# Kernel tuning notes

Measured on AMD Instinct MI355X. Metric: run time of the kernel, lower is better.

The kernel has to match this reference:

```python
import jax, jax.numpy as jnp
import numpy as np

N_NODES = 100000
N_EDGES = 1600000
D_IN, D_H, D_OUT = 128, 128, 64


def gcn_conv(x, src, dst, W, b, n_nodes):
    """PyG GCNConv (eval): x' = D^{-1/2} (A+I) D^{-1/2} X W + b.
    src/dst already include self-loops."""
    h = x @ W  # [N, d_out] -- transform first (fewer FLOPs when d_out <= d_in)
    deg = jax.ops.segment_sum(jnp.ones_like(dst, dtype=h.dtype), dst, num_segments=n_nodes)
    dinv = jnp.where(deg > 0, jax.lax.rsqrt(deg), 0.0)
    norm = dinv[src] * dinv[dst]  # [E]
    msg = h[src] * norm[:, None]  # gather + scale
    out = jax.ops.segment_sum(msg, dst, num_segments=n_nodes)  # scatter-add
    return out + b


def setup_inputs() -> dict:
    key = jax.random.key(0)
    k = jax.random.split(key, 8)
    x = jax.random.normal(k[0], (N_NODES, D_IN), dtype=jnp.float32)
    edge_index = jax.random.randint(k[1], (2, N_EDGES), 0, N_NODES, dtype=jnp.int32)
    s = 0.1
    W1 = jax.random.normal(k[2], (D_IN, D_H), dtype=jnp.float32) * s
    b1 = jnp.zeros((D_H,), dtype=jnp.float32)
    W2 = jax.random.normal(k[3], (D_H, D_H), dtype=jnp.float32) * s
    b2 = jnp.zeros((D_H,), dtype=jnp.float32)
    W3 = jax.random.normal(k[4], (D_H, D_OUT), dtype=jnp.float32) * s
    b3 = jnp.zeros((D_OUT,), dtype=jnp.float32)
    return {"x": x, "edge_index": edge_index, "W1": W1, "b1": b1,
            "W2": W2, "b2": b2, "W3": W3, "b3": b3}


def reference(x, edge_index, W1, b1, W2, b2, W3, b3):
    n = x.shape[0]
    # add self-loops once (shared by all layers)
    loops = jnp.arange(n, dtype=edge_index.dtype)
    src = jnp.concatenate([edge_index[0], loops])
    dst = jnp.concatenate([edge_index[1], loops])
    h = gcn_conv(x, src, dst, W1, b1, n)
    h = jax.nn.relu(h)  # dropout = identity in eval mode
    h = gcn_conv(h, src, dst, W2, b2, n)
    h = jax.nn.relu(h)
    out = gcn_conv(h, src, dst, W3, b3, n)
    return out
```

## Files before the change

### kernel.cpp

```cpp
#include <hip/hip_runtime.h>
#include <hip/hip_fp16.h>

#define N_NODES 100000
#define N_EDGES 1600000
#define NBUCKET 196
#define CAP     8960
#define EPB     6250

typedef _Float16 half8 __attribute__((ext_vector_type(8)));
typedef float float4v __attribute__((ext_vector_type(4)));

__launch_bounds__(256)
__global__ void k_partition(const int* __restrict__ src, const int* __restrict__ dst,
                            int* __restrict__ bcur, int* __restrict__ ebuf, int E) {
    __shared__ int hist[200];
    __shared__ int basebkt[200];
    const int tid = threadIdx.x;
    if (tid < 200) hist[tid] = 0;
    __syncthreads();
    const int e0 = blockIdx.x * EPB, e1 = min(e0 + EPB, E);
    for (int e = e0 + tid; e < e1; e += 256) atomicAdd(&hist[dst[e] >> 9], 1);
    __syncthreads();
    if (tid < NBUCKET) {
        int h = hist[tid];
        basebkt[tid] = tid * CAP + (h ? atomicAdd(&bcur[tid], h) : 0);
    }
    __syncthreads();
    if (tid < 200) hist[tid] = 0;
    __syncthreads();
    for (int e = e0 + tid; e < e1; e += 256) {
        int d = dst[e];
        int bk = d >> 9;
        int o = atomicAdd(&hist[bk], 1);
        ebuf[basebkt[bk] + o] = (src[e] << 9) | (d & 511);
    }
}

__launch_bounds__(256)
__global__ void k_bsort(const int* __restrict__ ebuf, const int* __restrict__ bcur,
                        int* __restrict__ adj, int* __restrict__ stv,
                        int* __restrict__ deg, float* __restrict__ dinv, int N) {
    __shared__ int cnt[512];
    __shared__ int offs[512];
    const int b = blockIdx.x;
    const int tid = threadIdx.x;
    const int base = b * CAP;
    const int n_b = min(bcur[b], CAP);
    const int node0 = b << 9;
    cnt[tid] = 0; cnt[tid + 256] = 0;
    __syncthreads();
    for (int i = tid; i < n_b; i += 256)
        atomicAdd(&cnt[ebuf[base + i] & 511], 1);
    __syncthreads();
    if (tid < 64) {
        int v[8], tot = 0;
#pragma unroll
        for (int j = 0; j < 8; ++j) { int t = cnt[tid * 8 + j]; v[j] = tot; tot += t; }
        int inc = tot;
#pragma unroll
        for (int d = 1; d < 64; d <<= 1) {
            int u = __shfl_up(inc, d, 64);
            if (tid >= d) inc += u;
        }
        const int excl = inc - tot;
#pragma unroll
        for (int j = 0; j < 8; ++j) offs[tid * 8 + j] = excl + v[j];
    }
    __syncthreads();
#pragma unroll
    for (int h = 0; h < 2; ++h) {
        int local = tid + h * 256;
        int node = node0 + local;
        if (node < N) {
            stv[node] = base + offs[local];
            deg[node] = cnt[local];
            dinv[node] = rsqrtf((float)(cnt[local] + 1));
        }
    }
    __syncthreads();
    for (int i = tid; i < n_b; i += 256) {
        int pk = ebuf[base + i];
        int pos = atomicAdd(&offs[pk & 511], 1);
        adj[base + pos] = pk >> 9;
    }
}

__global__ void k_wswz_all(const float* __restrict__ W1, const float* __restrict__ W2,
                           const float* __restrict__ W3, _Float16* __restrict__ wz1,
                           _Float16* __restrict__ wz2, _Float16* __restrict__ wz3,
                           int* __restrict__ bcur) {
    if (blockIdx.x == 0) bcur[threadIdx.x] = 0;
    int t = blockIdx.x * 256 + threadIdx.x;
    const float* W; _Float16* wsz; int BN;
    if (t < 2048)      { W = W1; wsz = wz1; BN = 128; }
    else if (t < 4096) { W = W2; wsz = wz2; BN = 128; t -= 2048; }
    else if (t < 5120) { W = W3; wsz = wz3; BN = 64;  t -= 4096; }
    else return;
    const int l = t & 63;
    const int kblk = (t >> 6) & 3;
    const int nt = t >> 8;
    const int krow = kblk * 32 + ((l >> 4) << 3);
    const int col = nt * 16 + (l & 15);
    _Float16 v[8];
#pragma unroll
    for (int j = 0; j < 8; ++j) v[j] = (_Float16)W[(krow + j) * BN + col];
    *(uint4*)&wsz[t << 3] = *(uint4*)v;
}

template <int BN, bool AFP16, int MINW>
__launch_bounds__(256, MINW)
__global__ void k_gemm_reg(const void* __restrict__ Xv, const _Float16* __restrict__ wsz,
                           const float* __restrict__ dinv, __half* __restrict__ out,
                           int N, int tiles) {
    constexpr int NT = BN / 16;
    const int lane = threadIdx.x & 63;
    const int q = lane >> 4;
    const int m = lane & 15;

    half8 wreg[NT * 4];
#pragma unroll
    for (int f = 0; f < NT * 4; ++f)
        wreg[f] = *(const half8*)&wsz[(f << 9) + (lane << 3)];

    const int wid = (blockIdx.x * 256 + threadIdx.x) >> 6;
    const int nw = gridDim.x * 4;

    for (int tile = wid; tile < tiles; tile += nw) {
        const int arow = tile * 16 + m;
        const int arowc = arow < N ? arow : N - 1;

        half8 xf[4];
        if constexpr (AFP16) {
            const _Float16* A = (const _Float16*)Xv + (size_t)arowc * 128 + (q << 3);
#pragma unroll
            for (int kb = 0; kb < 4; ++kb) xf[kb] = *(const half8*)(A + kb * 32);
        } else {
            const float* A = (const float*)Xv + (size_t)arowc * 128 + (q << 3);
#pragma unroll
            for (int kb = 0; kb < 4; ++kb) {
                float4 a0 = *(const float4*)(A + kb * 32);
                float4 a1 = *(const float4*)(A + kb * 32 + 4);
                xf[kb][0] = (_Float16)a0.x; xf[kb][1] = (_Float16)a0.y;
                xf[kb][2] = (_Float16)a0.z; xf[kb][3] = (_Float16)a0.w;
                xf[kb][4] = (_Float16)a1.x; xf[kb][5] = (_Float16)a1.y;
                xf[kb][6] = (_Float16)a1.z; xf[kb][7] = (_Float16)a1.w;
            }
        }

        float4v acc[NT];
#pragma unroll
        for (int nt = 0; nt < NT; ++nt) acc[nt] = (float4v){0.f, 0.f, 0.f, 0.f};
#pragma unroll
        for (int kb = 0; kb < 4; ++kb)
#pragma unroll
            for (int nt = 0; nt < NT; ++nt)
                acc[nt] = __builtin_amdgcn_mfma_f32_16x16x32_f16(wreg[nt * 4 + kb], xf[kb],
                                                                acc[nt], 0, 0, 0);

        if (arow < N) {
            const float s = dinv[arow];
#pragma unroll
            for (int nt = 0; nt < NT; ++nt) {
                _Float16 ov[4];
#pragma unroll
                for (int r = 0; r < 4; ++r) ov[r] = (_Float16)(acc[nt][r] * s);
                *(uint2*)&out[(size_t)arow * BN + nt * 16 + q * 4] = *(uint2*)ov;
            }
        }
    }
}

template <bool RELU>
__launch_bounds__(256)
__global__ void k_agg128(const __half* __restrict__ tp, const int* __restrict__ adj,
                         const int* __restrict__ startv, const int* __restrict__ deg,
                         const float* __restrict__ dinv, const float* __restrict__ bias,
                         _Float16* __restrict__ out, int N) {
    const int node = (blockIdx.x << 2) + (threadIdx.x >> 6);
    const int lane = threadIdx.x & 63;
    if (node >= N) return;
    const int s = startv[node];
    const int cnt = deg[node];
    const float di = dinv[node];
    const int g = lane >> 4;
    const int sl = lane & 15;
    const uint4* rowb = (const uint4*)tp;

    float acc[8] = {0.f, 0.f, 0.f, 0.f, 0.f, 0.f, 0.f, 0.f};
    auto addrow = [&](uint4 v) {
        float2 f0 = __half22float2(*(__half2*)&v.x);
        float2 f1 = __half22float2(*(__half2*)&v.y);
        float2 f2 = __half22float2(*(__half2*)&v.z);
        float2 f3 = __half22float2(*(__half2*)&v.w);
        acc[0] += f0.x; acc[1] += f0.y; acc[2] += f1.x; acc[3] += f1.y;
        acc[4] += f2.x; acc[5] += f2.y; acc[6] += f3.x; acc[7] += f3.y;
    };
    if (g == 0) addrow(rowb[(size_t)node * 16 + sl]);

    int e = 0;
    for (; e + 16 <= cnt; e += 16) {
        int j[4];
#pragma unroll
        for (int u = 0; u < 4; ++u) j[u] = adj[s + e + 4 * u + g];
        uint4 v[4];
#pragma unroll
        for (int u = 0; u < 4; ++u) v[u] = rowb[(size_t)j[u] * 16 + sl];
#pragma unroll
        for (int u = 0; u < 4; ++u) addrow(v[u]);
    }
    for (; e + 4 <= cnt; e += 4)
        addrow(rowb[(size_t)adj[s + e + g] * 16 + sl]);
    if (e + g < cnt)
        addrow(rowb[(size_t)adj[s + e + g] * 16 + sl]);

#pragma unroll
    for (int i = 0; i < 8; ++i) {
        acc[i] += __shfl_xor(acc[i], 32);
        acc[i] += __shfl_xor(acc[i], 16);
    }
    if (g == 0) {
        float4 b0 = *(const float4*)&bias[sl * 8];
        float4 b1 = *(const float4*)&bias[sl * 8 + 4];
        float o[8];
        o[0] = di * acc[0] + b0.x; o[1] = di * acc[1] + b0.y;
        o[2] = di * acc[2] + b0.z; o[3] = di * acc[3] + b0.w;
        o[4] = di * acc[4] + b1.x; o[5] = di * acc[5] + b1.y;
        o[6] = di * acc[6] + b1.z; o[7] = di * acc[7] + b1.w;
        if (RELU)
#pragma unroll
            for (int i = 0; i < 8; ++i) o[i] = fmaxf(o[i], 0.f);
        __half2 ov[4];
#pragma unroll
        for (int i = 0; i < 4; ++i) ov[i] = __floats2half2_rn(o[2 * i], o[2 * i + 1]);
        *(uint4*)&out[(size_t)node * 128 + sl * 8] = *(uint4*)ov;
    }
}

__launch_bounds__(256)
__global__ void k_agg64(const __half* __restrict__ tp, const int* __restrict__ adj,
                        const int* __restrict__ startv, const int* __restrict__ deg,
                        const float* __restrict__ dinv, const float* __restrict__ bias,
                        float* __restrict__ out, int N) {
    const int node = (blockIdx.x << 2) + (threadIdx.x >> 6);
    const int lane = threadIdx.x & 63;
    if (node >= N) return;
    const int s = startv[node];
    const int cnt = deg[node];
    const float di = dinv[node];
    const int g = lane >> 4;
    const int sl = lane & 15;
    const uint2* rowb = (const uint2*)tp;

    float acc[4] = {0.f, 0.f, 0.f, 0.f};
    auto addrow = [&](uint2 v) {
        float2 f0 = __half22float2(*(__half2*)&v.x);
        float2 f1 = __half22float2(*(__half2*)&v.y);
        acc[0] += f0.x; acc[1] += f0.y; acc[2] += f1.x; acc[3] += f1.y;
    };
    if (g == 0) addrow(rowb[(size_t)node * 16 + sl]);

    int e = 0;
    for (; e + 16 <= cnt; e += 16) {
        int j[4];
#pragma unroll
        for (int u = 0; u < 4; ++u) j[u] = adj[s + e + 4 * u + g];
        uint2 v[4];
#pragma unroll
        for (int u = 0; u < 4; ++u) v[u] = rowb[(size_t)j[u] * 16 + sl];
#pragma unroll
        for (int u = 0; u < 4; ++u) addrow(v[u]);
    }
    for (; e + 4 <= cnt; e += 4)
        addrow(rowb[(size_t)adj[s + e + g] * 16 + sl]);
    if (e + g < cnt)
        addrow(rowb[(size_t)adj[s + e + g] * 16 + sl]);

#pragma unroll
    for (int i = 0; i < 4; ++i) {
        acc[i] += __shfl_xor(acc[i], 32);
        acc[i] += __shfl_xor(acc[i], 16);
    }
    if (g == 0) {
        float4 bb = *(const float4*)&bias[sl * 4];
        float4 o;
        o.x = di * acc[0] + bb.x; o.y = di * acc[1] + bb.y;
        o.z = di * acc[2] + bb.z; o.w = di * acc[3] + bb.w;
        *(float4*)&out[(size_t)node * 64 + sl * 4] = o;
    }
}

extern "C" void kernel_launch(void* const* d_in, const int* in_sizes, int n_in,
                              void* d_out, int out_size, void* d_ws, size_t ws_size,
                              hipStream_t stream) {
    const float* x  = (const float*)d_in[0];
    const int*   ei = (const int*)d_in[1];
    const float* W1 = (const float*)d_in[2];
    const float* b1 = (const float*)d_in[3];
    const float* W2 = (const float*)d_in[4];
    const float* b2 = (const float*)d_in[5];
    const float* W3 = (const float*)d_in[6];
    const float* b3 = (const float*)d_in[7];
    float* out = (float*)d_out;
    const int* src = ei;
    const int* dst = ei + N_EDGES;

    char* p = (char*)d_ws;
    __half* tp      = (__half*)p;    p += (size_t)N_NODES * 128 * 2;
    _Float16* hbuf  = (_Float16*)p;  p += (size_t)N_NODES * 128 * 2;
    int*   deg  = (int*)p;    p += (size_t)N_NODES * 4;
    float* dinv = (float*)p;  p += (size_t)N_NODES * 4;
    int*   stv  = (int*)p;    p += (size_t)N_NODES * 4;
    int*   bCur = (int*)p;    p += 1024;
    int*   adj  = (int*)p;    p += (size_t)NBUCKET * CAP * 4 + 16384;
    _Float16* wz1 = (_Float16*)p; p += 16384 * 2;
    _Float16* wz2 = (_Float16*)p; p += 16384 * 2;
    _Float16* wz3 = (_Float16*)p; p += 8192 * 2;
    size_t need = (size_t)(p - (char*)d_ws);
    if (ws_size < need) return;

    int* ebuf = (int*)tp;

    k_wswz_all<<<20, 256, 0, stream>>>(W1, W2, W3, wz1, wz2, wz3, bCur);
    k_partition<<<256, 256, 0, stream>>>(src, dst, bCur, ebuf, N_EDGES);
    k_bsort<<<NBUCKET, 256, 0, stream>>>(ebuf, bCur, adj, stv, deg, dinv, N_NODES);

    const int tiles = (N_NODES + 15) / 16;
    const int ab = (N_NODES + 3) / 4;
    k_gemm_reg<128, false, 2><<<512, 256, 0, stream>>>(x, wz1, dinv, tp, N_NODES, tiles);
    k_agg128<true><<<ab, 256, 0, stream>>>(tp, adj, stv, deg, dinv, b1, hbuf, N_NODES);
    k_gemm_reg<128, true, 2><<<512, 256, 0, stream>>>(hbuf, wz2, dinv, tp, N_NODES, tiles);
    k_agg128<true><<<ab, 256, 0, stream>>>(tp, adj, stv, deg, dinv, b2, hbuf, N_NODES);
    k_gemm_reg<64, true, 4><<<1024, 256, 0, stream>>>(hbuf, wz3, dinv, tp, N_NODES, tiles);
    k_agg64<<<ab, 256, 0, stream>>>(tp, adj, stv, deg, dinv, b3, out, N_NODES);
}
```

Before: 367.9 us.

## Fuse all GCN stages into one persistent kernel with software grid barriers

Replaces the eight separate launches (weight swizzle, partition, bucket sort, three GEMMs, three aggregations) with a single persistent kernel of 1024 blocks. The stages are separated by a hierarchical atomic grid barrier, and the first GEMM overlaps with the bucket sort on the blocks left free. The source-side dinv scaling moves from the GEMM epilogue into the aggregation as a per-neighbor fma, which adds a dinv gather per edge. Weights are staged in LDS instead of registers. The change targets launch gaps and tail effects, but relies on all 1024 blocks being co-resident and a spin barrier with a timeout, which could deadlock or give wrong results if occupancy is insufficient.

```diff
diff --git a/kernel.cpp b/kernel.cpp
--- a/kernel.cpp
+++ b/kernel.cpp
@@ -5,130 +5,53 @@
 #define N_EDGES 1600000
 #define NBUCKET 196
 #define CAP     8960
-#define EPB     6250
+#define GRID    1024
+#define PBLK    (GRID - 20)
+#define EPB2    ((N_EDGES + PBLK - 1) / PBLK)
+#define NTILES  ((N_NODES + 15) / 16)
 
 typedef _Float16 half8 __attribute__((ext_vector_type(8)));
 typedef float float4v __attribute__((ext_vector_type(4)));
 
-__launch_bounds__(256)
-__global__ void k_partition(const int* __restrict__ src, const int* __restrict__ dst,
-                            int* __restrict__ bcur, int* __restrict__ ebuf, int E) {
-    __shared__ int hist[200];
-    __shared__ int basebkt[200];
+__device__ __forceinline__ void gridbar(int* bb, int phase) {
+    __syncthreads();
+    if (threadIdx.x == 0) {
+        __threadfence();
+        int g = blockIdx.x & 31;
+        if (atomicAdd(&bb[256 + phase * 32 + g], 1) == 31) {
+            if (atomicAdd(&bb[128 + phase * 16], 1) == 31) {
+                __threadfence();
+                atomicExch(&bb[phase * 16], 1);
+            }
+        }
+        long it = 0;
+        while (__hip_atomic_load(&bb[phase * 16], __ATOMIC_ACQUIRE,
+                                 __HIP_MEMORY_SCOPE_AGENT) == 0) {
+            __builtin_amdgcn_s_sleep(8);
+            if (++it > 1000000L) break;
+        }
+        __threadfence();
+    }
+    __syncthreads();
+}
+
+template <int BN, bool AFP16>
+__device__ __forceinline__ void gemm_phase(const void* Xv, const _Float16* wsz,
+                                           __half* out, _Float16* smem,
+                                           int bstart, int bcnt) {
+    if ((int)blockIdx.x < bstart) return;
     const int tid = threadIdx.x;
-    if (tid < 200) hist[tid] = 0;
+    for (int i = tid; i < BN * 16; i += 256)
+        *(uint4*)&smem[i << 3] = *(const uint4*)&wsz[i << 3];
     __syncthreads();
-    const int e0 = blockIdx.x * EPB, e1 = min(e0 + EPB, E);
-    for (int e = e0 + tid; e < e1; e += 256) atomicAdd(&hist[dst[e] >> 9], 1);
-    __syncthreads();
-    if (tid < NBUCKET) {
-        int h = hist[tid];
-        basebkt[tid] = tid * CAP + (h ? atomicAdd(&bcur[tid], h) : 0);
-    }
-    __syncthreads();
-    if (tid < 200) hist[tid] = 0;
-    __syncthreads();
-    for (int e = e0 + tid; e < e1; e += 256) {
-        int d = dst[e];
-        int bk = d >> 9;
-        int o = atomicAdd(&hist[bk], 1);
-        ebuf[basebkt[bk] + o] = (src[e] << 9) | (d & 511);
-    }
-}
-
-__launch_bounds__(256)
-__global__ void k_bsort(const int* __restrict__ ebuf, const int* __restrict__ bcur,
-                        int* __restrict__ adj, int* __restrict__ stv,
-                        int* __restrict__ deg, float* __restrict__ dinv, int N) {
-    __shared__ int cnt[512];
-    __shared__ int offs[512];
-    const int b = blockIdx.x;
-    const int tid = threadIdx.x;
-    const int base = b * CAP;
-    const int n_b = min(bcur[b], CAP);
-    const int node0 = b << 9;
-    cnt[tid] = 0; cnt[tid + 256] = 0;
-    __syncthreads();
-    for (int i = tid; i < n_b; i += 256)
-        atomicAdd(&cnt[ebuf[base + i] & 511], 1);
-    __syncthreads();
-    if (tid < 64) {
-        int v[8], tot = 0;
-#pragma unroll
-        for (int j = 0; j < 8; ++j) { int t = cnt[tid * 8 + j]; v[j] = tot; tot += t; }
-        int inc = tot;
-#pragma unroll
-        for (int d = 1; d < 64; d <<= 1) {
-            int u = __shfl_up(inc, d, 64);
-            if (tid >= d) inc += u;
-        }
-        const int excl = inc - tot;
-#pragma unroll
-        for (int j = 0; j < 8; ++j) offs[tid * 8 + j] = excl + v[j];
-    }
-    __syncthreads();
-#pragma unroll
-    for (int h = 0; h < 2; ++h) {
-        int local = tid + h * 256;
-        int node = node0 + local;
-        if (node < N) {
-            stv[node] = base + offs[local];
-            deg[node] = cnt[local];
-            dinv[node] = rsqrtf((float)(cnt[local] + 1));
-        }
-    }
-    __syncthreads();
-    for (int i = tid; i < n_b; i += 256) {
-        int pk = ebuf[base + i];
-        int pos = atomicAdd(&offs[pk & 511], 1);
-        adj[base + pos] = pk >> 9;
-    }
-}
-
-__global__ void k_wswz_all(const float* __restrict__ W1, const float* __restrict__ W2,
-                           const float* __restrict__ W3, _Float16* __restrict__ wz1,
-                           _Float16* __restrict__ wz2, _Float16* __restrict__ wz3,
-                           int* __restrict__ bcur) {
-    if (blockIdx.x == 0) bcur[threadIdx.x] = 0;
-    int t = blockIdx.x * 256 + threadIdx.x;
-    const float* W; _Float16* wsz; int BN;
-    if (t < 2048)      { W = W1; wsz = wz1; BN = 128; }
-    else if (t < 4096) { W = W2; wsz = wz2; BN = 128; t -= 2048; }
-    else if (t < 5120) { W = W3; wsz = wz3; BN = 64;  t -= 4096; }
-    else return;
-    const int l = t & 63;
-    const int kblk = (t >> 6) & 3;
-    const int nt = t >> 8;
-    const int krow = kblk * 32 + ((l >> 4) << 3);
-    const int col = nt * 16 + (l & 15);
-    _Float16 v[8];
-#pragma unroll
-    for (int j = 0; j < 8; ++j) v[j] = (_Float16)W[(krow + j) * BN + col];
-    *(uint4*)&wsz[t << 3] = *(uint4*)v;
-}
-
-template <int BN, bool AFP16, int MINW>
-__launch_bounds__(256, MINW)
-__global__ void k_gemm_reg(const void* __restrict__ Xv, const _Float16* __restrict__ wsz,
-                           const float* __restrict__ dinv, __half* __restrict__ out,
-                           int N, int tiles) {
-    constexpr int NT = BN / 16;
-    const int lane = threadIdx.x & 63;
+    const int lane = tid & 63;
     const int q = lane >> 4;
     const int m = lane & 15;
-
-    half8 wreg[NT * 4];
-#pragma unroll
-    for (int f = 0; f < NT * 4; ++f)
-        wreg[f] = *(const half8*)&wsz[(f << 9) + (lane << 3)];
-
-    const int wid = (blockIdx.x * 256 + threadIdx.x) >> 6;
-    const int nw = gridDim.x * 4;
-
-    for (int tile = wid; tile < tiles; tile += nw) {
+    const int wid = (((int)blockIdx.x - bstart) << 2) + (tid >> 6);
+    const int nw = bcnt << 2;
+    for (int tile = wid; tile < NTILES; tile += nw) {
         const int arow = tile * 16 + m;
-        const int arowc = arow < N ? arow : N - 1;
-
+        const int arowc = arow < N_NODES ? arow : N_NODES - 1;
         half8 xf[4];
         if constexpr (AFP16) {
             const _Float16* A = (const _Float16*)Xv + (size_t)arowc * 128 + (q << 3);
@@ -146,147 +69,223 @@
                 xf[kb][6] = (_Float16)a1.z; xf[kb][7] = (_Float16)a1.w;
             }
         }
-
+        constexpr int NT = BN / 16;
         float4v acc[NT];
 #pragma unroll
         for (int nt = 0; nt < NT; ++nt) acc[nt] = (float4v){0.f, 0.f, 0.f, 0.f};
 #pragma unroll
         for (int kb = 0; kb < 4; ++kb)
 #pragma unroll
-            for (int nt = 0; nt < NT; ++nt)
-                acc[nt] = __builtin_amdgcn_mfma_f32_16x16x32_f16(wreg[nt * 4 + kb], xf[kb],
-                                                                acc[nt], 0, 0, 0);
-
-        if (arow < N) {
-            const float s = dinv[arow];
+            for (int nt = 0; nt < NT; ++nt) {
+                half8 wf = *(const half8*)&smem[(((nt << 2) + kb) << 9) + (lane << 3)];
+                acc[nt] = __builtin_amdgcn_mfma_f32_16x16x32_f16(wf, xf[kb], acc[nt], 0, 0, 0);
+            }
+        if (arow < N_NODES) {
 #pragma unroll
             for (int nt = 0; nt < NT; ++nt) {
                 _Float16 ov[4];
 #pragma unroll
-                for (int r = 0; r < 4; ++r) ov[r] = (_Float16)(acc[nt][r] * s);
+                for (int r = 0; r < 4; ++r) ov[r] = (_Float16)acc[nt][r];
                 *(uint2*)&out[(size_t)arow * BN + nt * 16 + q * 4] = *(uint2*)ov;
             }
         }
     }
 }
 
-template <bool RELU>
-__launch_bounds__(256)
-__global__ void k_agg128(const __half* __restrict__ tp, const int* __restrict__ adj,
-                         const int* __restrict__ startv, const int* __restrict__ deg,
-                         const float* __restrict__ dinv, const float* __restrict__ bias,
-                         _Float16* __restrict__ out, int N) {
-    const int node = (blockIdx.x << 2) + (threadIdx.x >> 6);
+template <int D, bool RELU, typename OT>
+__device__ __forceinline__ void agg_phase(const __half* tp, const int* adj,
+                                          const int* stv, const int* deg,
+                                          const float* dinv, const float* bias,
+                                          OT* out) {
+    const int w = threadIdx.x >> 6;
     const int lane = threadIdx.x & 63;
-    if (node >= N) return;
-    const int s = startv[node];
-    const int cnt = deg[node];
-    const float di = dinv[node];
     const int g = lane >> 4;
     const int sl = lane & 15;
-    const uint4* rowb = (const uint4*)tp;
-
-    float acc[8] = {0.f, 0.f, 0.f, 0.f, 0.f, 0.f, 0.f, 0.f};
-    auto addrow = [&](uint4 v) {
-        float2 f0 = __half22float2(*(__half2*)&v.x);
-        float2 f1 = __half22float2(*(__half2*)&v.y);
-        float2 f2 = __half22float2(*(__half2*)&v.z);
-        float2 f3 = __half22float2(*(__half2*)&v.w);
-        acc[0] += f0.x; acc[1] += f0.y; acc[2] += f1.x; acc[3] += f1.y;
-        acc[4] += f2.x; acc[5] += f2.y; acc[6] += f3.x; acc[7] += f3.y;
-    };
-    if (g == 0) addrow(rowb[(size_t)node * 16 + sl]);
-
-    int e = 0;
-    for (; e + 16 <= cnt; e += 16) {
-        int j[4];
-#pragma unroll
-        for (int u = 0; u < 4; ++u) j[u] = adj[s + e + 4 * u + g];
-        uint4 v[4];
-#pragma unroll
-        for (int u = 0; u < 4; ++u) v[u] = rowb[(size_t)j[u] * 16 + sl];
-#pragma unroll
-        for (int u = 0; u < 4; ++u) addrow(v[u]);
-    }
-    for (; e + 4 <= cnt; e += 4)
-        addrow(rowb[(size_t)adj[s + e + g] * 16 + sl]);
-    if (e + g < cnt)
-        addrow(rowb[(size_t)adj[s + e + g] * 16 + sl]);
-
-#pragma unroll
-    for (int i = 0; i < 8; ++i) {
-        acc[i] += __shfl_xor(acc[i], 32);
-        acc[i] += __shfl_xor(acc[i], 16);
-    }
-    if (g == 0) {
-        float4 b0 = *(const float4*)&bias[sl * 8];
-        float4 b1 = *(const float4*)&bias[sl * 8 + 4];
-        float o[8];
-        o[0] = di * acc[0] + b0.x; o[1] = di * acc[1] + b0.y;
-        o[2] = di * acc[2] + b0.z; o[3] = di * acc[3] + b0.w;
-        o[4] = di * acc[4] + b1.x; o[5] = di * acc[5] + b1.y;
-        o[6] = di * acc[6] + b1.z; o[7] = di * acc[7] + b1.w;
-        if (RELU)
-#pragma unroll
-            for (int i = 0; i < 8; ++i) o[i] = fmaxf(o[i], 0.f);
-        __half2 ov[4];
-#pragma unroll
-        for (int i = 0; i < 4; ++i) ov[i] = __floats2half2_rn(o[2 * i], o[2 * i + 1]);
-        *(uint4*)&out[(size_t)node * 128 + sl * 8] = *(uint4*)ov;
-    }
-}
-
-__launch_bounds__(256)
-__global__ void k_agg64(const __half* __restrict__ tp, const int* __restrict__ adj,
-                        const int* __restrict__ startv, const int* __restrict__ deg,
-                        const float* __restrict__ dinv, const float* __restrict__ bias,
-                        float* __restrict__ out, int N) {
-    const int node = (blockIdx.x << 2) + (threadIdx.x >> 6);
-    const int lane = threadIdx.x & 63;
-    if (node >= N) return;
-    const int s = startv[node];
-    const int cnt = deg[node];
-    const float di = dinv[node];
-    const int g = lane >> 4;
-    const int sl = lane & 15;
-    const uint2* rowb = (const uint2*)tp;
-
-    float acc[4] = {0.f, 0.f, 0.f, 0.f};
-    auto addrow = [&](uint2 v) {
-        float2 f0 = __half22float2(*(__half2*)&v.x);
-        float2 f1 = __half22float2(*(__half2*)&v.y);
-        acc[0] += f0.x; acc[1] += f0.y; acc[2] += f1.x; acc[3] += f1.y;
-    };
-    if (g == 0) addrow(rowb[(size_t)node * 16 + sl]);
-
-    int e = 0;
-    for (; e + 16 <= cnt; e += 16) {
-        int j[4];
-#pragma unroll
-        for (int u = 0; u < 4; ++u) j[u] = adj[s + e + 4 * u + g];
-        uint2 v[4];
-#pragma unroll
-        for (int u = 0; u < 4; ++u) v[u] = rowb[(size_t)j[u] * 16 + sl];
-#pragma unroll
-        for (int u = 0; u < 4; ++u) addrow(v[u]);
-    }
-    for (; e + 4 <= cnt; e += 4)
-        addrow(rowb[(size_t)adj[s + e + g] * 16 + sl]);
-    if (e + g < cnt)
-        addrow(rowb[(size_t)adj[s + e + g] * 16 + sl]);
-
-#pragma unroll
-    for (int i = 0; i < 4; ++i) {
-        acc[i] += __shfl_xor(acc[i], 32);
-        acc[i] += __shfl_xor(acc[i], 16);
-    }
-    if (g == 0) {
-        float4 bb = *(const float4*)&bias[sl * 4];
-        float4 o;
-        o.x = di * acc[0] + bb.x; o.y = di * acc[1] + bb.y;
-        o.z = di * acc[2] + bb.z; o.w = di * acc[3] + bb.w;
-        *(float4*)&out[(size_t)node * 64 + sl * 4] = o;
-    }
+    constexpr int NA = D / 16;
+
+    for (int node = ((int)blockIdx.x << 2) + w; node < N_NODES; node += GRID * 4) {
+        const int s = stv[node];
+        const int cnt = deg[node];
+        const float di = dinv[node];
+        float acc[NA];
+#pragma unroll
+        for (int i = 0; i < NA; ++i) acc[i] = 0.f;
+
+        auto addrow = [&](float c, const __half2* v) {
+#pragma unroll
+            for (int i = 0; i < NA / 2; ++i) {
+                float2 f = __half22float2(v[i]);
+                acc[2 * i] = fmaf(c, f.x, acc[2 * i]);
+                acc[2 * i + 1] = fmaf(c, f.y, acc[2 * i + 1]);
+            }
+        };
+        const __half2* base = (const __half2*)tp;
+        if (g == 0) addrow(di, base + (size_t)node * (D / 2) + sl * (NA / 2));
+        int e = 0;
+        for (; e + 16 <= cnt; e += 16) {
+            int j[4];
+#pragma unroll
+            for (int u = 0; u < 4; ++u) j[u] = adj[s + e + 4 * u + g];
+            float dj[4];
+#pragma unroll
+            for (int u = 0; u < 4; ++u) dj[u] = dinv[j[u]];
+            __half2 v[4][NA / 2];
+#pragma unroll
+            for (int u = 0; u < 4; ++u)
+#pragma unroll
+                for (int i = 0; i < NA / 2; ++i)
+                    v[u][i] = base[(size_t)j[u] * (D / 2) + sl * (NA / 2) + i];
+#pragma unroll
+            for (int u = 0; u < 4; ++u) addrow(dj[u], v[u]);
+        }
+        for (; e + 4 <= cnt; e += 4) {
+            int j = adj[s + e + g];
+            addrow(dinv[j], base + (size_t)j * (D / 2) + sl * (NA / 2));
+        }
+        if (e + g < cnt) {
+            int j = adj[s + e + g];
+            addrow(dinv[j], base + (size_t)j * (D / 2) + sl * (NA / 2));
+        }
+#pragma unroll
+        for (int i = 0; i < NA; ++i) {
+            acc[i] += __shfl_xor(acc[i], 32);
+            acc[i] += __shfl_xor(acc[i], 16);
+        }
+        if (g == 0) {
+            float o[NA];
+#pragma unroll
+            for (int i = 0; i < NA; ++i) {
+                o[i] = di * acc[i] + bias[sl * NA + i];
+                if (RELU) o[i] = fmaxf(o[i], 0.f);
+            }
+            if constexpr (sizeof(OT) == 2) {
+                __half2 ov[NA / 2];
+#pragma unroll
+                for (int i = 0; i < NA / 2; ++i)
+                    ov[i] = __floats2half2_rn(o[2 * i], o[2 * i + 1]);
+                if constexpr (NA == 8)
+                    *(uint4*)&out[(size_t)node * D + sl * NA] = *(uint4*)ov;
+                else
+                    *(uint2*)&out[(size_t)node * D + sl * NA] = *(uint2*)ov;
+            } else {
+#pragma unroll
+                for (int i = 0; i < NA; i += 4)
+                    *(float4*)&out[(size_t)node * D + sl * NA + i] = *(float4*)&o[i];
+            }
+        }
+    }
+}
+
+__launch_bounds__(256, 4)
+__global__ void k_mega(const float* __restrict__ x, const int* __restrict__ src,
+                       const int* __restrict__ dst,
+                       const float* __restrict__ W1, const float* __restrict__ W2,
+                       const float* __restrict__ W3,
+                       const float* __restrict__ b1, const float* __restrict__ b2,
+                       const float* __restrict__ b3,
+                       int* bb, int* bCur, int* ebuf,
+                       _Float16* wz1, _Float16* wz2, _Float16* wz3,
+                       int* adj, int* stv, int* deg, float* dinv,
+                       __half* tp, _Float16* hbuf, float* out) {
+    __shared__ __align__(16) _Float16 smem[16384];
+    const int b = blockIdx.x;
+    const int tid = threadIdx.x;
+
+    if (b < 20) {
+        int t = b * 256 + tid;
+        const float* W; _Float16* wsz; int BN;
+        if (t < 2048)      { W = W1; wsz = wz1; BN = 128; }
+        else if (t < 4096) { W = W2; wsz = wz2; BN = 128; t -= 2048; }
+        else               { W = W3; wsz = wz3; BN = 64;  t -= 4096; }
+        const int l = t & 63;
+        const int kblk = (t >> 6) & 3;
+        const int nt = t >> 8;
+        const int krow = kblk * 32 + ((l >> 4) << 3);
+        const int col = nt * 16 + (l & 15);
+        _Float16 v[8];
+#pragma unroll
+        for (int j = 0; j < 8; ++j) v[j] = (_Float16)W[(krow + j) * BN + col];
+        *(uint4*)&wsz[t << 3] = *(uint4*)v;
+    } else {
+        int* hist = (int*)smem;
+        int* basebkt = hist + 256;
+        if (tid < 256) hist[tid] = 0;
+        __syncthreads();
+        const int e0 = (b - 20) * EPB2, e1 = min(e0 + EPB2, N_EDGES);
+        for (int e = e0 + tid; e < e1; e += 256) atomicAdd(&hist[dst[e] >> 9], 1);
+        __syncthreads();
+        if (tid < NBUCKET) {
+            int h = hist[tid];
+            basebkt[tid] = tid * CAP + (h ? atomicAdd(&bCur[tid], h) : 0);
+        }
+        __syncthreads();
+        if (tid < 256) hist[tid] = 0;
+        __syncthreads();
+        for (int e = e0 + tid; e < e1; e += 256) {
+            int d = dst[e];
+            int bk = d >> 9;
+            int o = atomicAdd(&hist[bk], 1);
+            ebuf[basebkt[bk] + o] = (src[e] << 9) | (d & 511);
+        }
+    }
+    gridbar(bb, 0);
+
+    if (b < NBUCKET) {
+        int* cnt = (int*)smem;
+        int* offs = cnt + 512;
+        const int base = b * CAP;
+        const int n_b = min(bCur[b], CAP);
+        const int node0 = b << 9;
+        cnt[tid] = 0; cnt[tid + 256] = 0;
+        __syncthreads();
+        for (int i = tid; i < n_b; i += 256)
+            atomicAdd(&cnt[ebuf[base + i] & 511], 1);
+        __syncthreads();
+        if (tid < 64) {
+            int v[8], tot = 0;
+#pragma unroll
+            for (int j = 0; j < 8; ++j) { int t = cnt[tid * 8 + j]; v[j] = tot; tot += t; }
+            int inc = tot;
+#pragma unroll
+            for (int d = 1; d < 64; d <<= 1) {
+                int u = __shfl_up(inc, d, 64);
+                if (tid >= d) inc += u;
+            }
+            const int excl = inc - tot;
+#pragma unroll
+            for (int j = 0; j < 8; ++j) offs[tid * 8 + j] = excl + v[j];
+        }
+        __syncthreads();
+#pragma unroll
+        for (int h = 0; h < 2; ++h) {
+            int local = tid + h * 256;
+            int node = node0 + local;
+            if (node < N_NODES) {
+                stv[node] = base + offs[local];
+                deg[node] = cnt[local];
+                dinv[node] = rsqrtf((float)(cnt[local] + 1));
+            }
+        }
+        __syncthreads();
+        for (int i = tid; i < n_b; i += 256) {
+            int pk = ebuf[base + i];
+            int pos = atomicAdd(&offs[pk & 511], 1);
+            adj[base + pos] = pk >> 9;
+        }
+    } else {
+        gemm_phase<128, false>(x, wz1, tp, smem, NBUCKET, GRID - NBUCKET);
+    }
+    gridbar(bb, 1);
+
+    agg_phase<128, true, _Float16>(tp, adj, stv, deg, dinv, b1, hbuf);
+    gridbar(bb, 2);
+    gemm_phase<128, true>(hbuf, wz2, tp, smem, 0, GRID);
+    gridbar(bb, 3);
+    agg_phase<128, true, _Float16>(tp, adj, stv, deg, dinv, b2, hbuf);
+    gridbar(bb, 4);
+    gemm_phase<64, true>(hbuf, wz3, tp, smem, 0, GRID);
+    gridbar(bb, 5);
+    agg_phase<64, false, float>(tp, adj, stv, deg, dinv, b3, out);
 }
 
 extern "C" void kernel_launch(void* const* d_in, const int* in_sizes, int n_in,
@@ -305,31 +304,23 @@
     const int* dst = ei + N_EDGES;
 
     char* p = (char*)d_ws;
+    int*  bb   = (int*)p;     p += 2048;
+    int*  bCur = (int*)p;     p += 2048;
     __half* tp      = (__half*)p;    p += (size_t)N_NODES * 128 * 2;
     _Float16* hbuf  = (_Float16*)p;  p += (size_t)N_NODES * 128 * 2;
     int*   deg  = (int*)p;    p += (size_t)N_NODES * 4;
     float* dinv = (float*)p;  p += (size_t)N_NODES * 4;
     int*   stv  = (int*)p;    p += (size_t)N_NODES * 4;
-    int*   bCur = (int*)p;    p += 1024;
     int*   adj  = (int*)p;    p += (size_t)NBUCKET * CAP * 4 + 16384;
+    int*   ebuf = (int*)p;    p += (size_t)NBUCKET * CAP * 4 + 16384;
     _Float16* wz1 = (_Float16*)p; p += 16384 * 2;
     _Float16* wz2 = (_Float16*)p; p += 16384 * 2;
     _Float16* wz3 = (_Float16*)p; p += 8192 * 2;
     size_t need = (size_t)(p - (char*)d_ws);
     if (ws_size < need) return;
 
-    int* ebuf = (int*)tp;
-
-    k_wswz_all<<<20, 256, 0, stream>>>(W1, W2, W3, wz1, wz2, wz3, bCur);
-    k_partition<<<256, 256, 0, stream>>>(src, dst, bCur, ebuf, N_EDGES);
-    k_bsort<<<NBUCKET, 256, 0, stream>>>(ebuf, bCur, adj, stv, deg, dinv, N_NODES);
-
-    const int tiles = (N_NODES + 15) / 16;
-    const int ab = (N_NODES + 3) / 4;
-    k_gemm_reg<128, false, 2><<<512, 256, 0, stream>>>(x, wz1, dinv, tp, N_NODES, tiles);
-    k_agg128<true><<<ab, 256, 0, stream>>>(tp, adj, stv, deg, dinv, b1, hbuf, N_NODES);
-    k_gemm_reg<128, true, 2><<<512, 256, 0, stream>>>(hbuf, wz2, dinv, tp, N_NODES, tiles);
-    k_agg128<true><<<ab, 256, 0, stream>>>(tp, adj, stv, deg, dinv, b2, hbuf, N_NODES);
-    k_gemm_reg<64, true, 4><<<1024, 256, 0, stream>>>(hbuf, wz3, dinv, tp, N_NODES, tiles);
-    k_agg64<<<ab, 256, 0, stream>>>(tp, adj, stv, deg, dinv, b3, out, N_NODES);
-}
+    hipMemsetAsync(d_ws, 0, 4096, stream);
+    k_mega<<<GRID, 256, 0, stream>>>(x, src, dst, W1, W2, W3, b1, b2, b3,
+                                     bb, bCur, ebuf, wz1, wz2, wz3,
+                                     adj, stv, deg, dinv, tp, hbuf, out);
+}
```

New measurement: 1.467 ms. +298.9%, slower.
